# Kernel optimization log

Measured on AMD Instinct MI355X. Metric: run time of the kernel, lower is better.

Reference implementation:

```python
import jax, jax.numpy as jnp
import numpy as np

N = 100000   # nodes
E = 1000000  # edges
G = 64       # graphs in batch
DIN, DH, DOUT = 128, 128, 64
BN_EPS = 1e-5


def setup_inputs() -> dict:
    key = jax.random.key(0)
    ks = jax.random.split(key, 20)
    inp = {}
    inp['x'] = jax.random.normal(ks[0], (N, DIN), dtype=jnp.float32)
    inp['edge_index'] = jax.random.randint(ks[1], (2, E), 0, N, dtype=jnp.int64)
    inp['batch'] = jnp.sort(jax.random.randint(ks[2], (N,), 0, G, dtype=jnp.int64))
    # GCN conv weights (stored [in, out]) + biases
    s = lambda k, i, o: jax.random.normal(k, (i, o), dtype=jnp.float32) / np.sqrt(i)
    inp['W1'] = s(ks[3], DIN, DH);  inp['b1'] = jnp.zeros((DH,), jnp.float32)
    inp['W2'] = s(ks[4], DH, DH);   inp['b2'] = jnp.zeros((DH,), jnp.float32)
    inp['W3'] = s(ks[5], DH, DOUT); inp['b3'] = jnp.zeros((DOUT,), jnp.float32)
    # BatchNorm params/buffers (eval mode)
    inp['g1'] = jnp.ones((DH,), jnp.float32);  inp['beta1'] = jnp.zeros((DH,), jnp.float32)
    inp['g2'] = jnp.ones((DH,), jnp.float32);  inp['beta2'] = jnp.zeros((DH,), jnp.float32)
    inp['mean1'] = jnp.zeros((DH,), jnp.float32); inp['var1'] = jnp.ones((DH,), jnp.float32)
    inp['mean2'] = jnp.zeros((DH,), jnp.float32); inp['var2'] = jnp.ones((DH,), jnp.float32)
    # GlobalAttention gate_nn: Linear(DOUT,DH) ReLU Linear(DH,1)
    inp['Wg1'] = s(ks[6], DOUT, DH); inp['bg1'] = jnp.zeros((DH,), jnp.float32)
    inp['Wg2'] = s(ks[7], DH, 1);    inp['bg2'] = jnp.zeros((1,), jnp.float32)
    # head MLP: Linear(DOUT,DH) ReLU Linear(DH,DOUT)
    inp['Wm1'] = s(ks[8], DOUT, DH); inp['bm1'] = jnp.zeros((DH,), jnp.float32)
    inp['Wm2'] = s(ks[9], DH, DOUT); inp['bm2'] = jnp.zeros((DOUT,), jnp.float32)
    return inp


def _gcn_conv(x, W, b, src, dst):
    # PyG GCNConv: add self-loops, sym-normalize, linear, scatter-sum, bias
    h = x @ W                                            # [N, out]
    deg = jnp.ones((N,), h.dtype).at[dst].add(1.0)       # in-degree + self-loop
    dinv = jax.lax.rsqrt(deg)
    norm = dinv[src] * dinv[dst]                         # [E]
    msg = h[src] * norm[:, None]                         # gather + scale
    out = jax.ops.segment_sum(msg, dst, num_segments=N)  # scatter
    out = out + h * (dinv * dinv)[:, None]               # self-loop term
    return out + b


def _bn(x, g, beta, mean, var):
    return (x - mean) * jax.lax.rsqrt(var + BN_EPS) * g + beta


def reference(x, edge_index, batch, W1, b1, W2, b2, W3, b3,
              g1, beta1, g2, beta2, mean1, var1, mean2, var2,
              Wg1, bg1, Wg2, bg2, Wm1, bm1, Wm2, bm2):
    src, dst = edge_index[0], edge_index[1]
    h = jax.nn.relu(_bn(_gcn_conv(x, W1, b1, src, dst), g1, beta1, mean1, var1))
    h = jax.nn.relu(_bn(_gcn_conv(h, W2, b2, src, dst), g2, beta2, mean2, var2))
    h = _gcn_conv(h, W3, b3, src, dst)                   # [N, DOUT]
    # GlobalAttention pooling: per-graph softmax of gate scores
    gate = jax.nn.relu(h @ Wg1 + bg1) @ Wg2 + bg2        # [N, 1]
    gate = gate[:, 0]
    m = jax.ops.segment_max(gate, batch, num_segments=G)
    e = jnp.exp(gate - m[batch])
    s = jax.ops.segment_sum(e, batch, num_segments=G)
    a = e / s[batch]                                     # [N]
    pooled = jax.ops.segment_sum(h * a[:, None], batch, num_segments=G)  # [G, DOUT]
    # MLP head (dropout off in eval)
    return jax.nn.relu(pooled @ Wm1 + bm1) @ Wm2 + bm2   # [G, DOUT]
```

## Files before the change

### kernel.cpp

```cpp
#include <hip/hip_runtime.h>
#include <hip/hip_bf16.h>
#include <hip/hip_fp16.h>
#include <math.h>

#define NN 100000
#define EE 1000000
#define GG 64
#define BN_EPS 1e-5f
#define CPB 16
#define EB 4096
#define NBLK ((EE + EB - 1) / EB)
#define NBUCK ((NN + 511) / 512)

typedef __attribute__((ext_vector_type(8))) short bf16x8;
typedef __attribute__((ext_vector_type(4))) float f32x4;

__device__ inline short f2bf(float f) {
  unsigned u = __float_as_uint(f);
  u = u + 0x7fff + ((u >> 16) & 1);
  return (short)(u >> 16);
}
__device__ inline float bf2f(short h) {
  return __uint_as_float(((unsigned)(unsigned short)h) << 16);
}

__device__ inline unsigned fenc(float f) {
  int b = __float_as_int(f);
  return (b < 0) ? ~(unsigned)b : ((unsigned)b | 0x80000000u);
}
__device__ inline float fdec(unsigned u) {
  int b = (u & 0x80000000u) ? (int)(u & 0x7fffffffu) : (int)~u;
  return __int_as_float(b);
}

__device__ inline void acc2(float& a0, float& a1, unsigned u) {
  asm("v_fma_mix_f32 %0, %2, 1.0, %0 op_sel:[0,0,0] op_sel_hi:[1,0,0]\n\t"
      "v_fma_mix_f32 %1, %2, 1.0, %1 op_sel:[1,0,0] op_sel_hi:[1,0,0]"
      : "+v"(a0), "+v"(a1)
      : "v"(u));
}
__device__ inline void acc8(float* a, uint4 u) {
  acc2(a[0], a[1], u.x);
  acc2(a[2], a[3], u.y);
  acc2(a[4], a[5], u.z);
  acc2(a[6], a[7], u.w);
}
__device__ inline uint4 zsel(uint4 u, int ok) {
  uint4 r;
  r.x = ok ? u.x : 0u;
  r.y = ok ? u.y : 0u;
  r.z = ok ? u.z : 0u;
  r.w = ok ? u.w : 0u;
  return r;
}

__global__ __launch_bounds__(256) void k_bhist(const int* __restrict__ dst,
                                               int* __restrict__ bhist, int E) {
  __shared__ int h[256];
  int t = threadIdx.x;
  h[t] = 0;
  __syncthreads();
  int base = blockIdx.x * EB;
#pragma unroll
  for (int j = 0; j < EB / 256; ++j) {
    int i = base + j * 256 + t;
    if (i < E) atomicAdd(&h[dst[i] >> 9], 1);
  }
  __syncthreads();
  bhist[blockIdx.x * 256 + t] = h[t];
}

__global__ __launch_bounds__(256) void k_bscan1(int* __restrict__ bhist,
                                                int* __restrict__ btot) {
  __shared__ int s[256];
  int bin = blockIdx.x, t = threadIdx.x;
  int v = (t < NBLK) ? bhist[t * 256 + bin] : 0;
  s[t] = v;
  __syncthreads();
  for (int o = 1; o < 256; o <<= 1) {
    int u = (t >= o) ? s[t - o] : 0;
    __syncthreads();
    s[t] += u;
    __syncthreads();
  }
  if (t < NBLK) bhist[t * 256 + bin] = s[t] - v;
  if (t == 255) btot[bin] = s[255];
}

__global__ __launch_bounds__(256) void k_bscan2(const int* __restrict__ btot,
                                                int* __restrict__ bstart) {
  __shared__ int s[256];
  int t = threadIdx.x;
  int v = btot[t];
  s[t] = v;
  __syncthreads();
  for (int o = 1; o < 256; o <<= 1) {
    int u = (t >= o) ? s[t - o] : 0;
    __syncthreads();
    s[t] += u;
    __syncthreads();
  }
  bstart[t] = s[t] - v;
}

__global__ __launch_bounds__(256) void k_bscat(const int* __restrict__ src,
                                               const int* __restrict__ dst,
                                               const int* __restrict__ bhist,
                                               const int* __restrict__ bstart,
                                               int2* __restrict__ pairs, int E) {
  __shared__ int h[256];
  __shared__ int base[256];
  int t = threadIdx.x;
  h[t] = 0;
  __syncthreads();
  int b0 = blockIdx.x * EB;
  int ds[EB / 256], rk[EB / 256];
#pragma unroll
  for (int j = 0; j < EB / 256; ++j) {
    int i = b0 + j * 256 + t;
    if (i < E) {
      int d = dst[i];
      ds[j] = d;
      rk[j] = atomicAdd(&h[d >> 9], 1);
    } else
      ds[j] = -1;
  }
  __syncthreads();
  base[t] = bstart[t] + bhist[blockIdx.x * 256 + t];
  __syncthreads();
#pragma unroll
  for (int j = 0; j < EB / 256; ++j) {
    int i = b0 + j * 256 + t;
    if (ds[j] >= 0) {
      int pos = base[ds[j] >> 9] + rk[j];
      pairs[pos] = make_int2(src[i], ds[j]);
    }
  }
}

__global__ __launch_bounds__(256) void k_bfill(const int2* __restrict__ pairs,
                                               const int* __restrict__ bstart,
                                               int* __restrict__ rowstart,
                                               int* __restrict__ eidx,
                                               float* __restrict__ dinv, int N,
                                               int E) {
  __shared__ int h[512];
  __shared__ int ex[512];
  __shared__ int ps[256];
  const int b = blockIdx.x;
  const int n0 = b << 9;
  const int e0 = bstart[b], e1 = bstart[b + 1];
  const int t = threadIdx.x;
  h[t] = 0;
  h[t + 256] = 0;
  __syncthreads();
  for (int i = e0 + t; i < e1; i += 256) atomicAdd(&h[pairs[i].y - n0], 1);
  __syncthreads();
  int v0 = h[2 * t], v1 = h[2 * t + 1];
  int sp = v0 + v1;
  ps[t] = sp;
  __syncthreads();
  for (int o = 1; o < 256; o <<= 1) {
    int u = (t >= o) ? ps[t - o] : 0;
    __syncthreads();
    ps[t] += u;
    __syncthreads();
  }
  int ex0 = ps[t] - sp;
  ex[2 * t] = ex0;
  ex[2 * t + 1] = ex0 + v0;
  __syncthreads();
  for (int i = t; i < 512; i += 256) {
    int node = n0 + i;
    if (node < N) {
      rowstart[node] = e0 + ex[i];
      dinv[node] = rsqrtf(1.0f + (float)h[i]);
    }
  }
  if (b == 0 && t == 0) rowstart[N] = E;
  __syncthreads();
  for (int i = e0 + t; i < e1; i += 256) {
    int2 p = pairs[i];
    int r = atomicAdd(&ex[p.y - n0], 1);
    eidx[e0 + r] = p.x;
  }
}

__global__ __launch_bounds__(256) void k_wsplit(const float* __restrict__ W1,
                                                const float* __restrict__ W2,
                                                const float* __restrict__ W3,
                                                const float* __restrict__ Wg1,
                                                short* __restrict__ wt) {
  int i = blockIdx.x * 256 + threadIdx.x;
  const float* W;
  short *hi, *lo;
  int K, M, idx;
  if (i < 16384) {
    W = W1; hi = wt; lo = wt + 16384; K = 128; M = 128; idx = i;
  } else if (i < 32768) {
    W = W2; hi = wt + 32768; lo = wt + 49152; K = 128; M = 128; idx = i - 16384;
  } else if (i < 40960) {
    W = W3; hi = wt + 65536; lo = wt + 73728; K = 128; M = 64; idx = i - 32768;
  } else {
    W = Wg1; hi = wt + 81920; lo = wt + 90112; K = 64; M = 128; idx = i - 40960;
  }
  int k = idx / M, n = idx % M;
  float w = W[idx];
  short h = f2bf(w);
  hi[n * K + k] = h;
  lo[n * K + k] = f2bf(w - bf2f(h));
}

__global__ __launch_bounds__(256) void k_bnprep(
    const float* __restrict__ g1, const float* __restrict__ b1,
    const float* __restrict__ m1, const float* __restrict__ v1,
    const float* __restrict__ g2, const float* __restrict__ b2,
    const float* __restrict__ m2, const float* __restrict__ v2,
    float* __restrict__ s1, float* __restrict__ h1, float* __restrict__ s2,
    float* __restrict__ h2) {
  int i = threadIdx.x;
  if (i < 128) {
    float s = g1[i] * rsqrtf(v1[i] + BN_EPS);
    s1[i] = s;
    h1[i] = b1[i] - m1[i] * s;
  } else {
    int j = i - 128;
    float s = g2[j] * rsqrtf(v2[j] + BN_EPS);
    s2[j] = s;
    h2[j] = b2[j] - m2[j] * s;
  }
}

template <int K, int M, int CTB, int AIN, int DINV, int GATE, int OUTH>
__device__ __forceinline__ void mgemm_body(
    short* lds, const float* __restrict__ Xf, const short* __restrict__ Xhi,
    const short* __restrict__ Xlo, const short* __restrict__ Wthi,
    const short* __restrict__ Wtlo, const float* __restrict__ dinv,
    const float* __restrict__ gbias, const float* __restrict__ Wg2v,
    const float* __restrict__ bg2v, void* __restrict__ Y,
    float* __restrict__ gate, int nrows) {
  constexpr int NC = K / 32;
  constexpr int KP = K + 8;
  constexpr int R = 2;
  const int lane = threadIdx.x & 63;
  const int wave = threadIdx.x >> 6;
  const int m16 = lane & 15;
  const int quad = lane >> 4;
  const int rowbase = blockIdx.x * 128 + wave * 32;
  const int cbase = blockIdx.y * CTB * 16;

  bf16x8 ahi[R][NC], alo[R][NC];
#pragma unroll
  for (int t = 0; t < R; ++t) {
    const int arow = rowbase + t * 16 + m16;
    const bool rok = arow < nrows;
#pragma unroll
    for (int c = 0; c < NC; ++c) {
      const int k0 = c * 32 + quad * 8;
      if constexpr (AIN) {
        if (rok) {
          ahi[t][c] = *(const bf16x8*)(Xhi + (size_t)arow * K + k0);
          alo[t][c] = *(const bf16x8*)(Xlo + (size_t)arow * K + k0);
        } else {
          ahi[t][c] = bf16x8{0, 0, 0, 0, 0, 0, 0, 0};
          alo[t][c] = bf16x8{0, 0, 0, 0, 0, 0, 0, 0};
        }
      } else {
        float4 v0 = make_float4(0.f, 0.f, 0.f, 0.f), v1 = v0;
        if (rok) {
          v0 = *(const float4*)(Xf + (size_t)arow * K + k0);
          v1 = *(const float4*)(Xf + (size_t)arow * K + k0 + 4);
        }
        float vv[8] = {v0.x, v0.y, v0.z, v0.w, v1.x, v1.y, v1.z, v1.w};
#pragma unroll
        for (int j = 0; j < 8; ++j) {
          short h = f2bf(vv[j]);
          ahi[t][c][j] = h;
          alo[t][c][j] = f2bf(vv[j] - bf2f(h));
        }
      }
    }
  }

  {
    constexpr int ELEMS = CTB * 16 * K;
#pragma unroll
    for (int i = threadIdx.x * 8; i < ELEMS; i += 256 * 8) {
      const int r = i / K, c = i % K;
      *(bf16x8*)(&lds[r * KP + c]) =
          *(const bf16x8*)(Wthi + (size_t)(cbase + r) * K + c);
      *(bf16x8*)(&lds[CTB * 16 * KP + r * KP + c]) =
          *(const bf16x8*)(Wtlo + (size_t)(cbase + r) * K + c);
    }
  }

  float dv[R][4];
  if constexpr (DINV && !GATE) {
#pragma unroll
    for (int t = 0; t < R; ++t)
#pragma unroll
      for (int r = 0; r < 4; ++r) {
        int row = rowbase + t * 16 + quad * 4 + r;
        dv[t][r] = (row < nrows) ? dinv[row] : 0.f;
      }
  }

  float gp[R][4];
  if constexpr (GATE) {
#pragma unroll
    for (int t = 0; t < R; ++t)
#pragma unroll
      for (int r = 0; r < 4; ++r) gp[t][r] = 0.f;
  }

  __syncthreads();

  f32x4 accs[CTB][R];
#pragma unroll
  for (int ct = 0; ct < CTB; ++ct) {
    bf16x8 bhi[NC], blo[NC];
    const int wrow = (ct * 16 + m16) * KP + quad * 8;
#pragma unroll
    for (int c = 0; c < NC; ++c) {
      bhi[c] = *(const bf16x8*)(&lds[wrow + c * 32]);
      blo[c] = *(const bf16x8*)(&lds[CTB * 16 * KP + wrow + c * 32]);
    }
#pragma unroll
    for (int t = 0; t < R; ++t) {
      f32x4 acc = {0.f, 0.f, 0.f, 0.f};
#pragma unroll
      for (int c = 0; c < NC; ++c) {
        acc = __builtin_amdgcn_mfma_f32_16x16x32_bf16(ahi[t][c], bhi[c], acc, 0, 0, 0);
        acc = __builtin_amdgcn_mfma_f32_16x16x32_bf16(ahi[t][c], blo[c], acc, 0, 0, 0);
        acc = __builtin_amdgcn_mfma_f32_16x16x32_bf16(alo[t][c], bhi[c], acc, 0, 0, 0);
      }
      if constexpr (GATE) {
        const int col = cbase + ct * 16 + m16;
        const float gb = gbias[col], wg = Wg2v[col];
#pragma unroll
        for (int r = 0; r < 4; ++r) gp[t][r] += fmaxf(acc[r] + gb, 0.f) * wg;
      } else {
        accs[ct][t] = acc;
      }
    }
  }

  if constexpr (GATE) {
#pragma unroll
    for (int o = 1; o < 16; o <<= 1) {
#pragma unroll
      for (int t = 0; t < R; ++t)
#pragma unroll
        for (int r = 0; r < 4; ++r) gp[t][r] += __shfl_xor(gp[t][r], o, 64);
    }
    if (m16 == 0) {
      const float b2 = bg2v[0];
#pragma unroll
      for (int t = 0; t < R; ++t)
#pragma unroll
        for (int r = 0; r < 4; ++r) {
          const int row = rowbase + t * 16 + quad * 4 + r;
          if (row < nrows) gate[row] = gp[t][r] + b2;
        }
    }
  } else {
    constexpr int COLS = CTB * 16;
    constexpr int SP = COLS + 8;
    __syncthreads();
#pragma unroll
    for (int ct = 0; ct < CTB; ++ct)
#pragma unroll
      for (int t = 0; t < R; ++t)
#pragma unroll
        for (int r = 0; r < 4; ++r) {
          const int row_l = wave * 32 + t * 16 + quad * 4 + r;
          float v = accs[ct][t][r];
          if constexpr (DINV) v *= dv[t][r];
          __half hv = __float2half(v);
          lds[row_l * SP + ct * 16 + m16] = *(short*)&hv;
        }
    __syncthreads();
    constexpr int TOT = 128 * COLS;
#pragma unroll
    for (int p = 0; p < TOT / (256 * 8); ++p) {
      const int idx8 = (p * 256 + threadIdx.x) * 8;
      const int row_l = idx8 / COLS;
      const int col0 = idx8 % COLS;
      const int grow = blockIdx.x * 128 + row_l;
      if (grow < nrows) {
        bf16x8 v = *(const bf16x8*)(&lds[row_l * SP + col0]);
        *(bf16x8*)((__half*)Y + (size_t)grow * M + cbase + col0) = v;
      }
    }
  }
}

#define MGEMM_ARGS                                                            \
  const float *Xf, const short *Xhi, const short *Xlo, const short *Wthi,     \
      const short *Wtlo, const float *dinv, const float *gbias,               \
      const float *Wg2v, const float *bg2v, void *Y, float *gate, int nrows

#define DEF_MGEMM(NAME, K, M, CTB, AIN, DINV, GATE, OUTH)                     \
  __global__ __launch_bounds__(256, 3) void NAME(MGEMM_ARGS) {                \
    __shared__ short lds[2 * CTB * 16 * (K + 8)];                             \
    mgemm_body<K, M, CTB, AIN, DINV, GATE, OUTH>(lds, Xf, Xhi, Xlo, Wthi,     \
                                                 Wtlo, dinv, gbias, Wg2v,     \
                                                 bg2v, Y, gate, nrows);       \
  }

DEF_MGEMM(k_mgemm1, 128, 128, 4, 0, 1, 0, 1)
DEF_MGEMM(k_mgemm2, 128, 128, 4, 1, 1, 0, 1)
DEF_MGEMM(k_mgemm3, 128, 64, 4, 1, 1, 0, 1)
DEF_MGEMM(k_mgemmg, 64, 128, 8, 0, 0, 1, 0)

template <int M, int EPI>
__device__ __forceinline__ void agg_body(
    const __half* __restrict__ hp, const int* __restrict__ rowstart,
    const int* __restrict__ eidx, const float* __restrict__ dinv,
    const float* __restrict__ bias, const float* __restrict__ bns,
    const float* __restrict__ bnh, float* __restrict__ outf,
    short* __restrict__ ohi, short* __restrict__ olo, int N) {
  constexpr int LPR = M / 8;
  constexpr int NPW = 64 / (2 * LPR);
  const int wv = (blockIdx.x * 256 + threadIdx.x) >> 6;
  const int lane = threadIdx.x & 63;
  const int grp = lane / (2 * LPR);
  const int slot = (lane / LPR) & 1;
  const int sub = lane % LPR;
  const int w = wv * NPW + grp;
  if (w >= N) return;
  const unsigned subo = (unsigned)sub * 16u;
  const float di = dinv[w];
  const int lo = rowstart[w], hi = rowstart[w + 1];
  const int hi1 = hi - 1;
  const char* hpb = (const char*)hp;
  float a[8] = {0.f, 0.f, 0.f, 0.f, 0.f, 0.f, 0.f, 0.f};

  int e = lo + slot;
  while (e < hi) {
    int idx[8], ss[8];
    uint4 uu[8];
#pragma unroll
    for (int p = 0; p < 8; ++p) {
      idx[p] = e + 2 * p;
      ss[p] = eidx[min(idx[p], hi1)];
    }
#pragma unroll
    for (int p = 0; p < 8; ++p)
      uu[p] = *(const uint4*)(hpb + ((unsigned)ss[p] * (unsigned)(M * 2) + subo));
#pragma unroll
    for (int p = 0; p < 8; ++p) {
      uu[p] = zsel(uu[p], idx[p] < hi);
      acc8(a, uu[p]);
    }
    e += 16;
  }
#pragma unroll
  for (int j = 0; j < 8; ++j) a[j] += __shfl_xor(a[j], LPR, 64);

  if (slot != 0) return;
  uint4 us = *(const uint4*)(hpb + ((unsigned)w * (unsigned)(M * 2) + subo));
  acc8(a, us);
  float4 b0 = *(const float4*)(bias + sub * 8);
  float4 b1 = *(const float4*)(bias + sub * 8 + 4);
  float r[8];
  r[0] = a[0] * di + b0.x;
  r[1] = a[1] * di + b0.y;
  r[2] = a[2] * di + b0.z;
  r[3] = a[3] * di + b0.w;
  r[4] = a[4] * di + b1.x;
  r[5] = a[5] * di + b1.y;
  r[6] = a[6] * di + b1.z;
  r[7] = a[7] * di + b1.w;
  if constexpr (EPI) {
    float4 s0 = *(const float4*)(bns + sub * 8);
    float4 s1 = *(const float4*)(bns + sub * 8 + 4);
    float4 h0 = *(const float4*)(bnh + sub * 8);
    float4 h1 = *(const float4*)(bnh + sub * 8 + 4);
    float sv[8] = {s0.x, s0.y, s0.z, s0.w, s1.x, s1.y, s1.z, s1.w};
    float hv[8] = {h0.x, h0.y, h0.z, h0.w, h1.x, h1.y, h1.z, h1.w};
    short hs[8], ls[8];
#pragma unroll
    for (int j = 0; j < 8; ++j) {
      float ev = fmaxf(r[j] * sv[j] + hv[j], 0.f);
      short hb = f2bf(ev);
      float res = ev - bf2f(hb);
      hs[j] = hb;
      ls[j] = (short)(__float_as_uint(res) >> 16);
    }
    *(short4*)(ohi + (size_t)w * M + sub * 8) = make_short4(hs[0], hs[1], hs[2], hs[3]);
    *(short4*)(ohi + (size_t)w * M + sub * 8 + 4) = make_short4(hs[4], hs[5], hs[6], hs[7]);
    *(short4*)(olo + (size_t)w * M + sub * 8) = make_short4(ls[0], ls[1], ls[2], ls[3]);
    *(short4*)(olo + (size_t)w * M + sub * 8 + 4) = make_short4(ls[4], ls[5], ls[6], ls[7]);
  } else {
    *(float4*)(outf + (size_t)w * M + sub * 8) = make_float4(r[0], r[1], r[2], r[3]);
    *(float4*)(outf + (size_t)w * M + sub * 8 + 4) = make_float4(r[4], r[5], r[6], r[7]);
  }
}

#define AGG_ARGS                                                              \
  const __half *hp, const int *rowstart, const int *eidx, const float *dinv,  \
      const float *bias, const float *bns, const float *bnh, float *outf,     \
      short *ohi, short *olo, int N

#define DEF_AGG(NAME, M, EPI)                                                 \
  __global__ __launch_bounds__(256) void NAME(AGG_ARGS) {                     \
    agg_body<M, EPI>(hp, rowstart, eidx, dinv, bias, bns, bnh, outf, ohi,     \
                     olo, N);                                                 \
  }

DEF_AGG(k_agg1, 128, 1)
DEF_AGG(k_agg2, 128, 1)
DEF_AGG(k_agg3, 64, 0)

__global__ __launch_bounds__(128) void k_gbounds(const int* __restrict__ batch,
                                                 int* __restrict__ gstart,
                                                 int N) {
  int g = threadIdx.x;
  if (g > GG) return;
  int lo = 0, hi = N;
  while (lo < hi) {
    int mid = (lo + hi) >> 1;
    if (batch[mid] < g) lo = mid + 1;
    else hi = mid;
  }
  gstart[g] = lo;
}

__global__ __launch_bounds__(256) void k_pmax(const float* __restrict__ gate,
                                              const int* __restrict__ gstart,
                                              unsigned* __restrict__ gmaxu) {
  __shared__ unsigned red[256];
  const int g = blockIdx.x / CPB;
  const int c = blockIdx.x % CPB;
  const int lo = gstart[g], hi = gstart[g + 1];
  const int len = hi - lo;
  const int b0 = lo + (int)(((long long)len * c) / CPB);
  const int b1 = lo + (int)(((long long)len * (c + 1)) / CPB);
  unsigned mx = 0u;
  for (int i = b0 + threadIdx.x; i < b1; i += 256) mx = max(mx, fenc(gate[i]));
  red[threadIdx.x] = mx;
  __syncthreads();
  for (int o = 128; o; o >>= 1) {
    if (threadIdx.x < o)
      red[threadIdx.x] = max(red[threadIdx.x], red[threadIdx.x + o]);
    __syncthreads();
  }
  if (threadIdx.x == 0 && red[0] != 0u) atomicMax(&gmaxu[g], red[0]);
}

__global__ __launch_bounds__(256) void k_psum(const float* __restrict__ gate,
                                              const float* __restrict__ h3,
                                              const unsigned* __restrict__ gmaxu,
                                              const int* __restrict__ gstart,
                                              float* __restrict__ pooledw,
                                              float* __restrict__ ssum) {
  __shared__ float accs[4][64];
  __shared__ float ses[4];
  const int g = blockIdx.x / CPB;
  const int c = blockIdx.x % CPB;
  const int lo = gstart[g], hi = gstart[g + 1];
  const int len = hi - lo;
  const int b0 = lo + (int)(((long long)len * c) / CPB);
  const int b1 = lo + (int)(((long long)len * (c + 1)) / CPB);
  const int wave = threadIdx.x >> 6, lane = threadIdx.x & 63;
  const float m = fdec(gmaxu[g]);
  float acc = 0.f, se = 0.f;
  for (int i = b0 + wave; i < b1; i += 4) {
    float e = expf(gate[i] - m);
    acc += e * h3[(size_t)i * 64 + lane];
    se += e;
  }
  accs[wave][lane] = acc;
  if (lane == 0) ses[wave] = se;
  __syncthreads();
  if (threadIdx.x < 64) {
    float a = accs[0][threadIdx.x] + accs[1][threadIdx.x] +
              accs[2][threadIdx.x] + accs[3][threadIdx.x];
    if (a != 0.f) atomicAdd(&pooledw[g * 64 + threadIdx.x], a);
  }
  if (threadIdx.x == 64) {
    float s = ses[0] + ses[1] + ses[2] + ses[3];
    if (s != 0.f) atomicAdd(&ssum[g], s);
  }
}

__global__ __launch_bounds__(256) void k_head(const float* __restrict__ pooledw,
                                              const float* __restrict__ ssum,
                                              const float* __restrict__ Wm1,
                                              const float* __restrict__ bm1,
                                              const float* __restrict__ Wm2,
                                              const float* __restrict__ bm2,
                                              float* __restrict__ out) {
  __shared__ float P[64 * 64];
  __shared__ float T[64 * 128];
  int tid = threadIdx.x;
  for (int i = tid; i < 4096; i += 256) {
    float s = ssum[i >> 6];
    P[i] = pooledw[i] * ((s > 0.f) ? 1.0f / s : 0.f);
  }
  __syncthreads();
  for (int e = tid; e < 8192; e += 256) {
    int r = e >> 7, c = e & 127;
    float a = bm1[c];
    for (int k = 0; k < 64; ++k) a += P[r * 64 + k] * Wm1[k * 128 + c];
    T[e] = fmaxf(a, 0.f);
  }
  __syncthreads();
  for (int e = tid; e < 4096; e += 256) {
    int r = e >> 6, c = e & 63;
    float a = bm2[c];
    for (int k = 0; k < 128; ++k) a += T[r * 128 + k] * Wm2[k * 64 + c];
    out[e] = a;
  }
}

extern "C" void kernel_launch(void* const* d_in, const int* in_sizes, int n_in,
                              void* d_out, int out_size, void* d_ws,
                              size_t ws_size, hipStream_t stream) {
  const int N = NN, E = EE;
  const float* x = (const float*)d_in[0];
  const int* ei = (const int*)d_in[1];
  const int* batch = (const int*)d_in[2];
  const float* W1 = (const float*)d_in[3];
  const float* b1 = (const float*)d_in[4];
  const float* W2 = (const float*)d_in[5];
  const float* b2 = (const float*)d_in[6];
  const float* W3 = (const float*)d_in[7];
  const float* b3 = (const float*)d_in[8];
  const float* g1 = (const float*)d_in[9];
  const float* beta1 = (const float*)d_in[10];
  const float* g2 = (const float*)d_in[11];
  const float* beta2 = (const float*)d_in[12];
  const float* mean1 = (const float*)d_in[13];
  const float* var1 = (const float*)d_in[14];
  const float* mean2 = (const float*)d_in[15];
  const float* var2 = (const float*)d_in[16];
  const float* Wg1 = (const float*)d_in[17];
  const float* bg1 = (const float*)d_in[18];
  const float* Wg2 = (const float*)d_in[19];
  const float* bg2 = (const float*)d_in[20];
  const float* Wm1 = (const float*)d_in[21];
  const float* bm1 = (const float*)d_in[22];
  const float* Wm2 = (const float*)d_in[23];
  const float* bm2 = (const float*)d_in[24];
  float* out = (float*)d_out;

  const int* src = ei;
  const int* dst = ei + E;

  char* wsb = (char*)d_ws;
  size_t off = 0;
  auto alloc = [&](size_t elems) -> void* {
    void* p = wsb + off;
    off += elems * 4;
    return p;
  };
  int* rowstart = (int*)alloc(N + 4);
  int* eidx = (int*)alloc(E);
  int2* pairs = (int2*)alloc((size_t)E * 2);
  int* bhist = (int*)alloc(NBLK * 256 + 256);
  int* btot = (int*)alloc(256);
  int* bstart = (int*)alloc(256);
  float* dinv = (float*)alloc(N);
  float* gate = (float*)alloc(N);
  __half* hbuf = (__half*)alloc((size_t)N * 64);
  short* ahi_p = (short*)alloc((size_t)N * 64);
  short* alo_p = (short*)alloc((size_t)N * 64);
  float* fbuf = (float*)alloc((size_t)N * 64);
  short* wt = (short*)alloc(49152);
  float* bn1s = (float*)alloc(128);
  float* bn1h = (float*)alloc(128);
  float* bn2s = (float*)alloc(128);
  float* bn2h = (float*)alloc(128);
  float* pooledw = (float*)alloc(GG * 64);
  float* ssum = (float*)alloc(GG);
  unsigned* gmaxu = (unsigned*)alloc(GG);
  int* gstart = (int*)alloc(GG + 4);
  (void)ws_size;
  (void)n_in;
  (void)in_sizes;
  (void)out_size;

  hipMemsetAsync(pooledw, 0, (GG * 64 + GG + GG) * sizeof(float), stream);
  k_bhist<<<NBLK, 256, 0, stream>>>(dst, bhist, E);
  k_bscan1<<<256, 256, 0, stream>>>(bhist, btot);
  k_bscan2<<<1, 256, 0, stream>>>(btot, bstart);
  k_bscat<<<NBLK, 256, 0, stream>>>(src, dst, bhist, bstart, pairs, E);
  k_bfill<<<NBUCK, 256, 0, stream>>>(pairs, bstart, rowstart, eidx, dinv, N, E);

  k_wsplit<<<192, 256, 0, stream>>>(W1, W2, W3, Wg1, wt);
  k_bnprep<<<1, 256, 0, stream>>>(g1, beta1, mean1, var1, g2, beta2, mean2,
                                  var2, bn1s, bn1h, bn2s, bn2h);
  k_gbounds<<<1, 128, 0, stream>>>(batch, gstart, N);

  const int gbb = (N + 127) / 128;
  const int ab128 = (N + 7) / 8;
  const int ab64 = (N + 15) / 16;

  k_mgemm1<<<dim3(gbb, 2), 256, 0, stream>>>(
      x, nullptr, nullptr, wt, wt + 16384, dinv, nullptr, nullptr, nullptr,
      hbuf, nullptr, N);
  k_agg1<<<ab128, 256, 0, stream>>>(hbuf, rowstart, eidx, dinv, b1, bn1s,
                                    bn1h, nullptr, ahi_p, alo_p, N);

  k_mgemm2<<<dim3(gbb, 2), 256, 0, stream>>>(
      nullptr, ahi_p, alo_p, wt + 32768, wt + 49152, dinv, nullptr, nullptr,
      nullptr, hbuf, nullptr, N);
  k_agg2<<<ab128, 256, 0, stream>>>(hbuf, rowstart, eidx, dinv, b2, bn2s,
                                    bn2h, nullptr, ahi_p, alo_p, N);

  k_mgemm3<<<dim3(gbb, 1), 256, 0, stream>>>(
      nullptr, ahi_p, alo_p, wt + 65536, wt + 73728, dinv, nullptr, nullptr,
      nullptr, hbuf, nullptr, N);
  k_agg3<<<ab64, 256, 0, stream>>>(hbuf, rowstart, eidx, dinv, b3, nullptr,
                                   nullptr, fbuf, nullptr, nullptr, N);

  k_mgemmg<<<dim3(gbb, 1), 256, 0, stream>>>(
      fbuf, nullptr, nullptr, wt + 81920, wt + 90112, nullptr, bg1, Wg2, bg2,
      nullptr, gate, N);

  k_pmax<<<GG * CPB, 256, 0, stream>>>(gate, gstart, gmaxu);
  k_psum<<<GG * CPB, 256, 0, stream>>>(gate, fbuf, gmaxu, gstart, pooledw,
                                       ssum);

  k_head<<<1, 256, 0, stream>>>(pooledw, ssum, Wm1, bm1, Wm2, bm2, out);
}
```

Measured before the change: 462.8 us.

## Fuse CSR build into cooperative kernel, merge prep kernels, persistent GEMM tiles

Merges the five CSR-construction kernels into one cooperative kernel that separates its phases with grid-wide syncs. The weight split, BN prep, graph-bounds search and pooled-buffer zeroing are folded into a single prep kernel, which also replaces the memset. The dense GEMMs become persistent: 768 blocks loop over row tiles, load the weight tile into LDS once, and prefetch the next A tile while the current tile's results are stored. The intent is to cut launch overhead and repeated weight loads, at the cost of grid-sync latency and a cooperative launch that requires all 256 blocks to be co-resident.

```diff
diff --git a/kernel.cpp b/kernel.cpp
--- a/kernel.cpp
+++ b/kernel.cpp
@@ -1,7 +1,10 @@
 #include <hip/hip_runtime.h>
 #include <hip/hip_bf16.h>
 #include <hip/hip_fp16.h>
+#include <hip/hip_cooperative_groups.h>
 #include <math.h>
+
+namespace cg = cooperative_groups;
 
 #define NN 100000
 #define EE 1000000
@@ -54,344 +57,365 @@
   return r;
 }
 
-__global__ __launch_bounds__(256) void k_bhist(const int* __restrict__ dst,
-                                               int* __restrict__ bhist, int E) {
-  __shared__ int h[256];
-  int t = threadIdx.x;
-  h[t] = 0;
-  __syncthreads();
-  int base = blockIdx.x * EB;
-#pragma unroll
-  for (int j = 0; j < EB / 256; ++j) {
-    int i = base + j * 256 + t;
-    if (i < E) atomicAdd(&h[dst[i] >> 9], 1);
-  }
-  __syncthreads();
-  bhist[blockIdx.x * 256 + t] = h[t];
-}
-
-__global__ __launch_bounds__(256) void k_bscan1(int* __restrict__ bhist,
-                                                int* __restrict__ btot) {
-  __shared__ int s[256];
-  int bin = blockIdx.x, t = threadIdx.x;
-  int v = (t < NBLK) ? bhist[t * 256 + bin] : 0;
-  s[t] = v;
-  __syncthreads();
-  for (int o = 1; o < 256; o <<= 1) {
-    int u = (t >= o) ? s[t - o] : 0;
-    __syncthreads();
-    s[t] += u;
-    __syncthreads();
-  }
-  if (t < NBLK) bhist[t * 256 + bin] = s[t] - v;
-  if (t == 255) btot[bin] = s[255];
-}
-
-__global__ __launch_bounds__(256) void k_bscan2(const int* __restrict__ btot,
-                                                int* __restrict__ bstart) {
-  __shared__ int s[256];
-  int t = threadIdx.x;
-  int v = btot[t];
-  s[t] = v;
-  __syncthreads();
-  for (int o = 1; o < 256; o <<= 1) {
-    int u = (t >= o) ? s[t - o] : 0;
-    __syncthreads();
-    s[t] += u;
-    __syncthreads();
-  }
-  bstart[t] = s[t] - v;
-}
-
-__global__ __launch_bounds__(256) void k_bscat(const int* __restrict__ src,
-                                               const int* __restrict__ dst,
-                                               const int* __restrict__ bhist,
-                                               const int* __restrict__ bstart,
-                                               int2* __restrict__ pairs, int E) {
-  __shared__ int h[256];
-  __shared__ int base[256];
-  int t = threadIdx.x;
-  h[t] = 0;
-  __syncthreads();
-  int b0 = blockIdx.x * EB;
-  int ds[EB / 256], rk[EB / 256];
-#pragma unroll
-  for (int j = 0; j < EB / 256; ++j) {
-    int i = b0 + j * 256 + t;
-    if (i < E) {
-      int d = dst[i];
-      ds[j] = d;
-      rk[j] = atomicAdd(&h[d >> 9], 1);
-    } else
-      ds[j] = -1;
-  }
-  __syncthreads();
-  base[t] = bstart[t] + bhist[blockIdx.x * 256 + t];
-  __syncthreads();
-#pragma unroll
-  for (int j = 0; j < EB / 256; ++j) {
-    int i = b0 + j * 256 + t;
-    if (ds[j] >= 0) {
-      int pos = base[ds[j] >> 9] + rk[j];
-      pairs[pos] = make_int2(src[i], ds[j]);
-    }
-  }
-}
-
-__global__ __launch_bounds__(256) void k_bfill(const int2* __restrict__ pairs,
-                                               const int* __restrict__ bstart,
-                                               int* __restrict__ rowstart,
-                                               int* __restrict__ eidx,
-                                               float* __restrict__ dinv, int N,
-                                               int E) {
+__global__ __launch_bounds__(256) void k_csr(const int* __restrict__ src,
+                                             const int* __restrict__ dst,
+                                             int* __restrict__ bhist,
+                                             int* __restrict__ btot,
+                                             int* __restrict__ bstart,
+                                             int2* __restrict__ pairs,
+                                             int* __restrict__ rowstart,
+                                             int* __restrict__ eidx,
+                                             float* __restrict__ dinv, int N,
+                                             int E) {
+  cg::grid_group grid = cg::this_grid();
   __shared__ int h[512];
   __shared__ int ex[512];
   __shared__ int ps[256];
+  const int t = threadIdx.x;
   const int b = blockIdx.x;
-  const int n0 = b << 9;
-  const int e0 = bstart[b], e1 = bstart[b + 1];
-  const int t = threadIdx.x;
-  h[t] = 0;
-  h[t + 256] = 0;
-  __syncthreads();
-  for (int i = e0 + t; i < e1; i += 256) atomicAdd(&h[pairs[i].y - n0], 1);
-  __syncthreads();
-  int v0 = h[2 * t], v1 = h[2 * t + 1];
-  int sp = v0 + v1;
-  ps[t] = sp;
-  __syncthreads();
-  for (int o = 1; o < 256; o <<= 1) {
-    int u = (t >= o) ? ps[t - o] : 0;
-    __syncthreads();
-    ps[t] += u;
-    __syncthreads();
-  }
-  int ex0 = ps[t] - sp;
-  ex[2 * t] = ex0;
-  ex[2 * t + 1] = ex0 + v0;
-  __syncthreads();
-  for (int i = t; i < 512; i += 256) {
-    int node = n0 + i;
-    if (node < N) {
-      rowstart[node] = e0 + ex[i];
-      dinv[node] = rsqrtf(1.0f + (float)h[i]);
-    }
-  }
-  if (b == 0 && t == 0) rowstart[N] = E;
-  __syncthreads();
-  for (int i = e0 + t; i < e1; i += 256) {
-    int2 p = pairs[i];
-    int r = atomicAdd(&ex[p.y - n0], 1);
-    eidx[e0 + r] = p.x;
-  }
-}
-
-__global__ __launch_bounds__(256) void k_wsplit(const float* __restrict__ W1,
-                                                const float* __restrict__ W2,
-                                                const float* __restrict__ W3,
-                                                const float* __restrict__ Wg1,
-                                                short* __restrict__ wt) {
-  int i = blockIdx.x * 256 + threadIdx.x;
-  const float* W;
-  short *hi, *lo;
-  int K, M, idx;
-  if (i < 16384) {
-    W = W1; hi = wt; lo = wt + 16384; K = 128; M = 128; idx = i;
-  } else if (i < 32768) {
-    W = W2; hi = wt + 32768; lo = wt + 49152; K = 128; M = 128; idx = i - 16384;
-  } else if (i < 40960) {
-    W = W3; hi = wt + 65536; lo = wt + 73728; K = 128; M = 64; idx = i - 32768;
+
+  if (b < NBLK) {
+    h[t] = 0;
+    __syncthreads();
+    int base = b * EB;
+#pragma unroll
+    for (int j = 0; j < EB / 256; ++j) {
+      int i = base + j * 256 + t;
+      if (i < E) atomicAdd(&h[dst[i] >> 9], 1);
+    }
+    __syncthreads();
+    bhist[b * 256 + t] = h[t];
+  }
+  grid.sync();
+
+  {
+    int v = (t < NBLK) ? bhist[t * 256 + b] : 0;
+    ps[t] = v;
+    __syncthreads();
+    for (int o = 1; o < 256; o <<= 1) {
+      int u = (t >= o) ? ps[t - o] : 0;
+      __syncthreads();
+      ps[t] += u;
+      __syncthreads();
+    }
+    if (t < NBLK) bhist[t * 256 + b] = ps[t] - v;
+    if (t == 255) btot[b] = ps[255];
+  }
+  grid.sync();
+
+  if (b == 0) {
+    int v = btot[t];
+    ps[t] = v;
+    __syncthreads();
+    for (int o = 1; o < 256; o <<= 1) {
+      int u = (t >= o) ? ps[t - o] : 0;
+      __syncthreads();
+      ps[t] += u;
+      __syncthreads();
+    }
+    bstart[t] = ps[t] - v;
+  }
+  grid.sync();
+
+  if (b < NBLK) {
+    h[t] = 0;
+    __syncthreads();
+    int b0 = b * EB;
+    int ds_[EB / 256], rk[EB / 256];
+#pragma unroll
+    for (int j = 0; j < EB / 256; ++j) {
+      int i = b0 + j * 256 + t;
+      if (i < E) {
+        int d = dst[i];
+        ds_[j] = d;
+        rk[j] = atomicAdd(&h[d >> 9], 1);
+      } else
+        ds_[j] = -1;
+    }
+    __syncthreads();
+    ex[t] = bstart[t] + bhist[b * 256 + t];
+    __syncthreads();
+#pragma unroll
+    for (int j = 0; j < EB / 256; ++j) {
+      int i = b0 + j * 256 + t;
+      if (ds_[j] >= 0) pairs[ex[ds_[j] >> 9] + rk[j]] = make_int2(src[i], ds_[j]);
+    }
+  }
+  grid.sync();
+
+  if (b < NBUCK) {
+    const int n0 = b << 9;
+    const int e0 = bstart[b], e1 = bstart[b + 1];
+    h[t] = 0;
+    h[t + 256] = 0;
+    __syncthreads();
+    for (int i = e0 + t; i < e1; i += 256) atomicAdd(&h[pairs[i].y - n0], 1);
+    __syncthreads();
+    int v0 = h[2 * t], v1 = h[2 * t + 1];
+    int sp = v0 + v1;
+    ps[t] = sp;
+    __syncthreads();
+    for (int o = 1; o < 256; o <<= 1) {
+      int u = (t >= o) ? ps[t - o] : 0;
+      __syncthreads();
+      ps[t] += u;
+      __syncthreads();
+    }
+    int ex0 = ps[t] - sp;
+    ex[2 * t] = ex0;
+    ex[2 * t + 1] = ex0 + v0;
+    __syncthreads();
+    for (int i = t; i < 512; i += 256) {
+      int node = n0 + i;
+      if (node < N) {
+        rowstart[node] = e0 + ex[i];
+        dinv[node] = rsqrtf(1.0f + (float)h[i]);
+      }
+    }
+    if (b == 0 && t == 0) rowstart[N] = E;
+    __syncthreads();
+    for (int i = e0 + t; i < e1; i += 256) {
+      int2 p = pairs[i];
+      int r = atomicAdd(&ex[p.y - n0], 1);
+      eidx[e0 + r] = p.x;
+    }
+  }
+}
+
+__global__ __launch_bounds__(256) void k_prep(
+    const float* __restrict__ W1, const float* __restrict__ W2,
+    const float* __restrict__ W3, const float* __restrict__ Wg1,
+    short* __restrict__ wt, const float* __restrict__ g1,
+    const float* __restrict__ b1, const float* __restrict__ m1,
+    const float* __restrict__ v1, const float* __restrict__ g2,
+    const float* __restrict__ b2, const float* __restrict__ m2,
+    const float* __restrict__ v2, float* __restrict__ s1,
+    float* __restrict__ h1, float* __restrict__ s2, float* __restrict__ h2,
+    const int* __restrict__ batch, int* __restrict__ gstart,
+    float* __restrict__ pooledw, int N) {
+  const int b = blockIdx.x, t = threadIdx.x;
+  if (b < 192) {
+    int i = b * 256 + t;
+    const float* W;
+    short *hi, *lo;
+    int K, M, idx;
+    if (i < 16384) {
+      W = W1; hi = wt; lo = wt + 16384; K = 128; M = 128; idx = i;
+    } else if (i < 32768) {
+      W = W2; hi = wt + 32768; lo = wt + 49152; K = 128; M = 128; idx = i - 16384;
+    } else if (i < 40960) {
+      W = W3; hi = wt + 65536; lo = wt + 73728; K = 128; M = 64; idx = i - 32768;
+    } else {
+      W = Wg1; hi = wt + 81920; lo = wt + 90112; K = 64; M = 128; idx = i - 40960;
+    }
+    int k = idx / M, n = idx % M;
+    float w = W[idx];
+    short h = f2bf(w);
+    hi[n * K + k] = h;
+    lo[n * K + k] = f2bf(w - bf2f(h));
+  } else if (b == 192) {
+    if (t < 128) {
+      float s = g1[t] * rsqrtf(v1[t] + BN_EPS);
+      s1[t] = s;
+      h1[t] = b1[t] - m1[t] * s;
+    } else {
+      int j = t - 128;
+      float s = g2[j] * rsqrtf(v2[j] + BN_EPS);
+      s2[j] = s;
+      h2[j] = b2[j] - m2[j] * s;
+    }
   } else {
-    W = Wg1; hi = wt + 81920; lo = wt + 90112; K = 64; M = 128; idx = i - 40960;
-  }
-  int k = idx / M, n = idx % M;
-  float w = W[idx];
-  short h = f2bf(w);
-  hi[n * K + k] = h;
-  lo[n * K + k] = f2bf(w - bf2f(h));
-}
-
-__global__ __launch_bounds__(256) void k_bnprep(
-    const float* __restrict__ g1, const float* __restrict__ b1,
-    const float* __restrict__ m1, const float* __restrict__ v1,
-    const float* __restrict__ g2, const float* __restrict__ b2,
-    const float* __restrict__ m2, const float* __restrict__ v2,
-    float* __restrict__ s1, float* __restrict__ h1, float* __restrict__ s2,
-    float* __restrict__ h2) {
-  int i = threadIdx.x;
-  if (i < 128) {
-    float s = g1[i] * rsqrtf(v1[i] + BN_EPS);
-    s1[i] = s;
-    h1[i] = b1[i] - m1[i] * s;
-  } else {
-    int j = i - 128;
-    float s = g2[j] * rsqrtf(v2[j] + BN_EPS);
-    s2[j] = s;
-    h2[j] = b2[j] - m2[j] * s;
+    if (t <= GG) {
+      int lo = 0, hi = N;
+      while (lo < hi) {
+        int mid = (lo + hi) >> 1;
+        if (batch[mid] < t) lo = mid + 1;
+        else hi = mid;
+      }
+      gstart[t] = lo;
+    }
+    for (int i = t; i < GG * 64 + GG + GG; i += 256) pooledw[i] = 0.f;
   }
 }
 
 template <int K, int M, int CTB, int AIN, int DINV, int GATE, int OUTH>
 __device__ __forceinline__ void mgemm_body(
-    short* lds, const float* __restrict__ Xf, const short* __restrict__ Xhi,
-    const short* __restrict__ Xlo, const short* __restrict__ Wthi,
-    const short* __restrict__ Wtlo, const float* __restrict__ dinv,
-    const float* __restrict__ gbias, const float* __restrict__ Wg2v,
-    const float* __restrict__ bg2v, void* __restrict__ Y,
-    float* __restrict__ gate, int nrows) {
+    short* wlds, short* slds, const float* __restrict__ Xf,
+    const short* __restrict__ Xhi, const short* __restrict__ Xlo,
+    const short* __restrict__ Wthi, const short* __restrict__ Wtlo,
+    const float* __restrict__ dinv, const float* __restrict__ gbias,
+    const float* __restrict__ Wg2v, const float* __restrict__ bg2v,
+    void* __restrict__ Y, float* __restrict__ gate, int nrows) {
   constexpr int NC = K / 32;
   constexpr int KP = K + 8;
   constexpr int R = 2;
+  constexpr int COLS = CTB * 16;
+  constexpr int SP = COLS + 8;
+  constexpr int NY = M / COLS;
   const int lane = threadIdx.x & 63;
   const int wave = threadIdx.x >> 6;
   const int m16 = lane & 15;
   const int quad = lane >> 4;
-  const int rowbase = blockIdx.x * 128 + wave * 32;
-  const int cbase = blockIdx.y * CTB * 16;
+  const int nb = gridDim.x / NY;
+  const int y = blockIdx.x / nb;
+  const int b0 = blockIdx.x % nb;
+  const int cbase = y * COLS;
+  const int ntiles = (nrows + 127) >> 7;
+
+  {
+    constexpr int ELEMS = CTB * 16 * K;
+    for (int i = threadIdx.x * 8; i < ELEMS; i += 256 * 8) {
+      const int r = i / K, c = i % K;
+      *(bf16x8*)(&wlds[r * KP + c]) =
+          *(const bf16x8*)(Wthi + (size_t)(cbase + r) * K + c);
+      *(bf16x8*)(&wlds[CTB * 16 * KP + r * KP + c]) =
+          *(const bf16x8*)(Wtlo + (size_t)(cbase + r) * K + c);
+    }
+  }
 
   bf16x8 ahi[R][NC], alo[R][NC];
-#pragma unroll
-  for (int t = 0; t < R; ++t) {
-    const int arow = rowbase + t * 16 + m16;
-    const bool rok = arow < nrows;
-#pragma unroll
-    for (int c = 0; c < NC; ++c) {
-      const int k0 = c * 32 + quad * 8;
-      if constexpr (AIN) {
-        if (rok) {
-          ahi[t][c] = *(const bf16x8*)(Xhi + (size_t)arow * K + k0);
-          alo[t][c] = *(const bf16x8*)(Xlo + (size_t)arow * K + k0);
+  auto loadA = [&](int tl) {
+#pragma unroll
+    for (int t = 0; t < R; ++t) {
+      const int arow = tl * 128 + wave * 32 + t * 16 + m16;
+      const bool rok = arow < nrows;
+#pragma unroll
+      for (int c = 0; c < NC; ++c) {
+        const int k0 = c * 32 + quad * 8;
+        if constexpr (AIN) {
+          if (rok) {
+            ahi[t][c] = *(const bf16x8*)(Xhi + (size_t)arow * K + k0);
+            alo[t][c] = *(const bf16x8*)(Xlo + (size_t)arow * K + k0);
+          } else {
+            ahi[t][c] = bf16x8{0, 0, 0, 0, 0, 0, 0, 0};
+            alo[t][c] = bf16x8{0, 0, 0, 0, 0, 0, 0, 0};
+          }
         } else {
-          ahi[t][c] = bf16x8{0, 0, 0, 0, 0, 0, 0, 0};
-          alo[t][c] = bf16x8{0, 0, 0, 0, 0, 0, 0, 0};
-        }
-      } else {
-        float4 v0 = make_float4(0.f, 0.f, 0.f, 0.f), v1 = v0;
-        if (rok) {
-          v0 = *(const float4*)(Xf + (size_t)arow * K + k0);
-          v1 = *(const float4*)(Xf + (size_t)arow * K + k0 + 4);
-        }
-        float vv[8] = {v0.x, v0.y, v0.z, v0.w, v1.x, v1.y, v1.z, v1.w};
-#pragma unroll
-        for (int j = 0; j < 8; ++j) {
-          short h = f2bf(vv[j]);
-          ahi[t][c][j] = h;
-          alo[t][c][j] = f2bf(vv[j] - bf2f(h));
+          float4 v0 = make_float4(0.f, 0.f, 0.f, 0.f), v1 = v0;
+          if (rok) {
+            v0 = *(const float4*)(Xf + (size_t)arow * K + k0);
+            v1 = *(const float4*)(Xf + (size_t)arow * K + k0 + 4);
+          }
+          float vv[8] = {v0.x, v0.y, v0.z, v0.w, v1.x, v1.y, v1.z, v1.w};
+#pragma unroll
+          for (int j = 0; j < 8; ++j) {
+            short h = f2bf(vv[j]);
+            ahi[t][c][j] = h;
+            alo[t][c][j] = f2bf(vv[j] - bf2f(h));
+          }
         }
       }
     }
-  }
-
-  {
-    constexpr int ELEMS = CTB * 16 * K;
-#pragma unroll
-    for (int i = threadIdx.x * 8; i < ELEMS; i += 256 * 8) {
-      const int r = i / K, c = i % K;
-      *(bf16x8*)(&lds[r * KP + c]) =
-          *(const bf16x8*)(Wthi + (size_t)(cbase + r) * K + c);
-      *(bf16x8*)(&lds[CTB * 16 * KP + r * KP + c]) =
-          *(const bf16x8*)(Wtlo + (size_t)(cbase + r) * K + c);
-    }
-  }
-
-  float dv[R][4];
-  if constexpr (DINV && !GATE) {
-#pragma unroll
-    for (int t = 0; t < R; ++t)
-#pragma unroll
-      for (int r = 0; r < 4; ++r) {
-        int row = rowbase + t * 16 + quad * 4 + r;
-        dv[t][r] = (row < nrows) ? dinv[row] : 0.f;
+  };
+
+  int tile = b0;
+  if (tile < ntiles) loadA(tile);
+  __syncthreads();
+
+  while (tile < ntiles) {
+    const int rowbase = tile * 128 + wave * 32;
+
+    float dv[R][4];
+    if constexpr (DINV && !GATE) {
+#pragma unroll
+      for (int t = 0; t < R; ++t)
+#pragma unroll
+        for (int r = 0; r < 4; ++r) {
+          int row = rowbase + t * 16 + quad * 4 + r;
+          dv[t][r] = (row < nrows) ? dinv[row] : 0.f;
+        }
+    }
+
+    float gp[R][4];
+    if constexpr (GATE) {
+#pragma unroll
+      for (int t = 0; t < R; ++t)
+#pragma unroll
+        for (int r = 0; r < 4; ++r) gp[t][r] = 0.f;
+    }
+
+    f32x4 accs[CTB][R];
+#pragma unroll
+    for (int ct = 0; ct < CTB; ++ct) {
+      bf16x8 bhi[NC], blo[NC];
+      const int wrow = (ct * 16 + m16) * KP + quad * 8;
+#pragma unroll
+      for (int c = 0; c < NC; ++c) {
+        bhi[c] = *(const bf16x8*)(&wlds[wrow + c * 32]);
+        blo[c] = *(const bf16x8*)(&wlds[CTB * 16 * KP + wrow + c * 32]);
       }
-  }
-
-  float gp[R][4];
-  if constexpr (GATE) {
-#pragma unroll
-    for (int t = 0; t < R; ++t)
-#pragma unroll
-      for (int r = 0; r < 4; ++r) gp[t][r] = 0.f;
-  }
-
-  __syncthreads();
-
-  f32x4 accs[CTB][R];
-#pragma unroll
-  for (int ct = 0; ct < CTB; ++ct) {
-    bf16x8 bhi[NC], blo[NC];
-    const int wrow = (ct * 16 + m16) * KP + quad * 8;
-#pragma unroll
-    for (int c = 0; c < NC; ++c) {
-      bhi[c] = *(const bf16x8*)(&lds[wrow + c * 32]);
-      blo[c] = *(const bf16x8*)(&lds[CTB * 16 * KP + wrow + c * 32]);
-    }
-#pragma unroll
-    for (int t = 0; t < R; ++t) {
-      f32x4 acc = {0.f, 0.f, 0.f, 0.f};
-#pragma unroll
-      for (int c = 0; c < NC; ++c) {
-        acc = __builtin_amdgcn_mfma_f32_16x16x32_bf16(ahi[t][c], bhi[c], acc, 0, 0, 0);
-        acc = __builtin_amdgcn_mfma_f32_16x16x32_bf16(ahi[t][c], blo[c], acc, 0, 0, 0);
-        acc = __builtin_amdgcn_mfma_f32_16x16x32_bf16(alo[t][c], bhi[c], acc, 0, 0, 0);
+#pragma unroll
+      for (int t = 0; t < R; ++t) {
+        f32x4 acc = {0.f, 0.f, 0.f, 0.f};
+#pragma unroll
+        for (int c = 0; c < NC; ++c) {
+          acc = __builtin_amdgcn_mfma_f32_16x16x32_bf16(ahi[t][c], bhi[c], acc, 0, 0, 0);
+          acc = __builtin_amdgcn_mfma_f32_16x16x32_bf16(ahi[t][c], blo[c], acc, 0, 0, 0);
+          acc = __builtin_amdgcn_mfma_f32_16x16x32_bf16(alo[t][c], bhi[c], acc, 0, 0, 0);
+        }
+        if constexpr (GATE) {
+          const int col = cbase + ct * 16 + m16;
+          const float gb = gbias[col], wg = Wg2v[col];
+#pragma unroll
+          for (int r = 0; r < 4; ++r) gp[t][r] += fmaxf(acc[r] + gb, 0.f) * wg;
+        } else {
+          accs[ct][t] = acc;
+        }
       }
-      if constexpr (GATE) {
-        const int col = cbase + ct * 16 + m16;
-        const float gb = gbias[col], wg = Wg2v[col];
-#pragma unroll
-        for (int r = 0; r < 4; ++r) gp[t][r] += fmaxf(acc[r] + gb, 0.f) * wg;
-      } else {
-        accs[ct][t] = acc;
+    }
+
+    const int next = tile + nb;
+    if (next < ntiles) loadA(next);
+
+    if constexpr (GATE) {
+#pragma unroll
+      for (int o = 1; o < 16; o <<= 1) {
+#pragma unroll
+        for (int t = 0; t < R; ++t)
+#pragma unroll
+          for (int r = 0; r < 4; ++r) gp[t][r] += __shfl_xor(gp[t][r], o, 64);
       }
-    }
-  }
-
-  if constexpr (GATE) {
-#pragma unroll
-    for (int o = 1; o < 16; o <<= 1) {
-#pragma unroll
-      for (int t = 0; t < R; ++t)
-#pragma unroll
-        for (int r = 0; r < 4; ++r) gp[t][r] += __shfl_xor(gp[t][r], o, 64);
-    }
-    if (m16 == 0) {
-      const float b2 = bg2v[0];
-#pragma unroll
-      for (int t = 0; t < R; ++t)
-#pragma unroll
-        for (int r = 0; r < 4; ++r) {
-          const int row = rowbase + t * 16 + quad * 4 + r;
-          if (row < nrows) gate[row] = gp[t][r] + b2;
+      if (m16 == 0) {
+        const float b2 = bg2v[0];
+#pragma unroll
+        for (int t = 0; t < R; ++t)
+#pragma unroll
+          for (int r = 0; r < 4; ++r) {
+            const int row = rowbase + t * 16 + quad * 4 + r;
+            if (row < nrows) gate[row] = gp[t][r] + b2;
+          }
+      }
+    } else {
+      asm volatile("s_waitcnt lgkmcnt(0)" ::: "memory");
+      __builtin_amdgcn_s_barrier();
+#pragma unroll
+      for (int ct = 0; ct < CTB; ++ct)
+#pragma unroll
+        for (int t = 0; t < R; ++t)
+#pragma unroll
+          for (int r = 0; r < 4; ++r) {
+            const int row_l = wave * 32 + t * 16 + quad * 4 + r;
+            float v = accs[ct][t][r];
+            if constexpr (DINV) v *= dv[t][r];
+            __half hv = __float2half(v);
+            slds[row_l * SP + ct * 16 + m16] = *(short*)&hv;
+          }
+      asm volatile("s_waitcnt lgkmcnt(0)" ::: "memory");
+      __builtin_amdgcn_s_barrier();
+      constexpr int TOT = 128 * COLS;
+#pragma unroll
+      for (int p = 0; p < TOT / (256 * 8); ++p) {
+        const int idx8 = (p * 256 + threadIdx.x) * 8;
+        const int row_l = idx8 / COLS;
+        const int col0 = idx8 % COLS;
+        const int grow = tile * 128 + row_l;
+        if (grow < nrows) {
+          bf16x8 v = *(const bf16x8*)(&slds[row_l * SP + col0]);
+          *(bf16x8*)((__half*)Y + (size_t)grow * M + cbase + col0) = v;
         }
-    }
-  } else {
-    constexpr int COLS = CTB * 16;
-    constexpr int SP = COLS + 8;
-    __syncthreads();
-#pragma unroll
-    for (int ct = 0; ct < CTB; ++ct)
-#pragma unroll
-      for (int t = 0; t < R; ++t)
-#pragma unroll
-        for (int r = 0; r < 4; ++r) {
-          const int row_l = wave * 32 + t * 16 + quad * 4 + r;
-          float v = accs[ct][t][r];
-          if constexpr (DINV) v *= dv[t][r];
-          __half hv = __float2half(v);
-          lds[row_l * SP + ct * 16 + m16] = *(short*)&hv;
-        }
-    __syncthreads();
-    constexpr int TOT = 128 * COLS;
-#pragma unroll
-    for (int p = 0; p < TOT / (256 * 8); ++p) {
-      const int idx8 = (p * 256 + threadIdx.x) * 8;
-      const int row_l = idx8 / COLS;
-      const int col0 = idx8 % COLS;
-      const int grow = blockIdx.x * 128 + row_l;
-      if (grow < nrows) {
-        bf16x8 v = *(const bf16x8*)(&lds[row_l * SP + col0]);
-        *(bf16x8*)((__half*)Y + (size_t)grow * M + cbase + col0) = v;
       }
     }
+    tile = next;
   }
 }
 
@@ -402,10 +426,11 @@
 
 #define DEF_MGEMM(NAME, K, M, CTB, AIN, DINV, GATE, OUTH)                     \
   __global__ __launch_bounds__(256, 3) void NAME(MGEMM_ARGS) {                \
-    __shared__ short lds[2 * CTB * 16 * (K + 8)];                             \
-    mgemm_body<K, M, CTB, AIN, DINV, GATE, OUTH>(lds, Xf, Xhi, Xlo, Wthi,     \
-                                                 Wtlo, dinv, gbias, Wg2v,     \
-                                                 bg2v, Y, gate, nrows);       \
+    __shared__ short wlds[2 * CTB * 16 * (K + 8)];                            \
+    __shared__ short slds[GATE ? 8 : 128 * (CTB * 16 + 8)];                   \
+    mgemm_body<K, M, CTB, AIN, DINV, GATE, OUTH>(wlds, slds, Xf, Xhi, Xlo,    \
+                                                 Wthi, Wtlo, dinv, gbias,     \
+                                                 Wg2v, bg2v, Y, gate, nrows); \
   }
 
 DEF_MGEMM(k_mgemm1, 128, 128, 4, 0, 1, 0, 1)
@@ -512,20 +537,6 @@
 DEF_AGG(k_agg1, 128, 1)
 DEF_AGG(k_agg2, 128, 1)
 DEF_AGG(k_agg3, 64, 0)
-
-__global__ __launch_bounds__(128) void k_gbounds(const int* __restrict__ batch,
-                                                 int* __restrict__ gstart,
-                                                 int N) {
-  int g = threadIdx.x;
-  if (g > GG) return;
-  int lo = 0, hi = N;
-  while (lo < hi) {
-    int mid = (lo + hi) >> 1;
-    if (batch[mid] < g) lo = mid + 1;
-    else hi = mid;
-  }
-  gstart[g] = lo;
-}
 
 __global__ __launch_bounds__(256) void k_pmax(const float* __restrict__ gate,
                                               const int* __restrict__ gstart,
@@ -682,43 +693,44 @@
   (void)in_sizes;
   (void)out_size;
 
-  hipMemsetAsync(pooledw, 0, (GG * 64 + GG + GG) * sizeof(float), stream);
-  k_bhist<<<NBLK, 256, 0, stream>>>(dst, bhist, E);
-  k_bscan1<<<256, 256, 0, stream>>>(bhist, btot);
-  k_bscan2<<<1, 256, 0, stream>>>(btot, bstart);
-  k_bscat<<<NBLK, 256, 0, stream>>>(src, dst, bhist, bstart, pairs, E);
-  k_bfill<<<NBUCK, 256, 0, stream>>>(pairs, bstart, rowstart, eidx, dinv, N, E);
-
-  k_wsplit<<<192, 256, 0, stream>>>(W1, W2, W3, Wg1, wt);
-  k_bnprep<<<1, 256, 0, stream>>>(g1, beta1, mean1, var1, g2, beta2, mean2,
-                                  var2, bn1s, bn1h, bn2s, bn2h);
-  k_gbounds<<<1, 128, 0, stream>>>(batch, gstart, N);
-
-  const int gbb = (N + 127) / 128;
+  {
+    int nN = N, nE = E;
+    void* cargs[] = {(void*)&src,   (void*)&dst,  (void*)&bhist,
+                     (void*)&btot,  (void*)&bstart, (void*)&pairs,
+                     (void*)&rowstart, (void*)&eidx, (void*)&dinv,
+                     (void*)&nN,    (void*)&nE};
+    hipLaunchCooperativeKernel((void*)k_csr, dim3(256), dim3(256), cargs, 0,
+                               stream);
+  }
+
+  k_prep<<<194, 256, 0, stream>>>(W1, W2, W3, Wg1, wt, g1, beta1, mean1, var1,
+                                  g2, beta2, mean2, var2, bn1s, bn1h, bn2s,
+                                  bn2h, batch, gstart, pooledw, N);
+
+  const int PG = 768;
   const int ab128 = (N + 7) / 8;
   const int ab64 = (N + 15) / 16;
 
-  k_mgemm1<<<dim3(gbb, 2), 256, 0, stream>>>(
-      x, nullptr, nullptr, wt, wt + 16384, dinv, nullptr, nullptr, nullptr,
-      hbuf, nullptr, N);
+  k_mgemm1<<<PG, 256, 0, stream>>>(x, nullptr, nullptr, wt, wt + 16384, dinv,
+                                   nullptr, nullptr, nullptr, hbuf, nullptr, N);
   k_agg1<<<ab128, 256, 0, stream>>>(hbuf, rowstart, eidx, dinv, b1, bn1s,
                                     bn1h, nullptr, ahi_p, alo_p, N);
 
-  k_mgemm2<<<dim3(gbb, 2), 256, 0, stream>>>(
-      nullptr, ahi_p, alo_p, wt + 32768, wt + 49152, dinv, nullptr, nullptr,
-      nullptr, hbuf, nullptr, N);
+  k_mgemm2<<<PG, 256, 0, stream>>>(nullptr, ahi_p, alo_p, wt + 32768,
+                                   wt + 49152, dinv, nullptr, nullptr, nullptr,
+                                   hbuf, nullptr, N);
   k_agg2<<<ab128, 256, 0, stream>>>(hbuf, rowstart, eidx, dinv, b2, bn2s,
                                     bn2h, nullptr, ahi_p, alo_p, N);
 
-  k_mgemm3<<<dim3(gbb, 1), 256, 0, stream>>>(
-      nullptr, ahi_p, alo_p, wt + 65536, wt + 73728, dinv, nullptr, nullptr,
-      nullptr, hbuf, nullptr, N);
+  k_mgemm3<<<PG, 256, 0, stream>>>(nullptr, ahi_p, alo_p, wt + 65536,
+                                   wt + 73728, dinv, nullptr, nullptr, nullptr,
+                                   hbuf, nullptr, N);
   k_agg3<<<ab64, 256, 0, stream>>>(hbuf, rowstart, eidx, dinv, b3, nullptr,
                                    nullptr, fbuf, nullptr, nullptr, N);
 
-  k_mgemmg<<<dim3(gbb, 1), 256, 0, stream>>>(
-      fbuf, nullptr, nullptr, wt + 81920, wt + 90112, nullptr, bg1, Wg2, bg2,
-      nullptr, gate, N);
+  k_mgemmg<<<PG, 256, 0, stream>>>(fbuf, nullptr, nullptr, wt + 81920,
+                                   wt + 90112, nullptr, bg1, Wg2, bg2, nullptr,
+                                   gate, N);
 
   k_pmax<<<GG * CPB, 256, 0, stream>>>(gate, gstart, gmaxu);
   k_psum<<<GG * CPB, 256, 0, stream>>>(gate, fbuf, gmaxu, gstart, pooledw,
```

New measurement: 639.0 us. +38.1%, slower.
